# Optimization experiments

Measured on AMD Instinct MI355X. Metric: run time of the kernel, lower is better.

Reference implementation:

```python
import jax, jax.numpy as jnp
import numpy as np

N, E, G, ND, H, C, L = 100000, 640000, 1000, 128, 128, 10, 4
ATOMS_PER_GRAPH = 100  # N = G * ATOMS_PER_GRAPH
NEG_SLOPE = 0.01  # nn.LeakyReLU default


def setup_inputs() -> dict:
    key = jax.random.key(0)
    ks = jax.random.split(key, 16)
    s = 0.05
    return {
        "node_attr": jax.random.normal(ks[0], (N, ND), jnp.float32),
        "edge_index": jax.random.randint(ks[1], (2, E), 0, N, jnp.int64),
        "num_atoms": jnp.full((G,), ATOMS_PER_GRAPH, dtype=jnp.int64),
        "enc_W": jax.random.normal(ks[2], (ND, H), jnp.float32) * s,
        "enc_b": jnp.zeros((H,), jnp.float32),
        "gcn_W": jax.random.normal(ks[3], (L, H, H), jnp.float32) * s,
        "gcn_b": jnp.zeros((L, H), jnp.float32),
        "r_W1": jax.random.normal(ks[4], (H, H), jnp.float32) * s,
        "r_b1": jnp.zeros((H,), jnp.float32),
        "r_W2": jax.random.normal(ks[5], (H, H), jnp.float32) * s,
        "r_b2": jnp.zeros((H,), jnp.float32),
        "s_W1": jax.random.normal(ks[6], (H, H), jnp.float32) * s,
        "s_b1": jnp.zeros((H,), jnp.float32),
        "s_W2": jax.random.normal(ks[7], (H, H), jnp.float32) * s,
        "s_b2": jnp.zeros((H,), jnp.float32),
        "fin_W": jax.random.normal(ks[8], (H, C), jnp.float32) * s,
        "fin_b": jnp.zeros((C,), jnp.float32),
    }


def _leaky(x):
    return jnp.where(x > 0, x, NEG_SLOPE * x)


def reference(node_attr, edge_index, num_atoms, enc_W, enc_b, gcn_W, gcn_b,
              r_W1, r_b1, r_W2, r_b2, s_W1, s_b1, s_W2, s_b2, fin_W, fin_b):
    dst, src = edge_index[0], edge_index[1]
    # degree normalization constant across layers: deg(i) = in-edge count, divide by deg+1
    deg = jax.ops.segment_sum(jnp.ones((E,), node_attr.dtype), dst, num_segments=N)
    inv_deg = 1.0 / (deg + 1.0)  # [N]

    x = node_attr @ enc_W + enc_b  # [N, H]
    for l in range(L):
        h = x @ gcn_W[l] + gcn_b[l]
        agg = jax.ops.segment_sum(h[src], dst, num_segments=N)  # scatter_sum over dst
        x = (h + agg) * inv_deg[:, None]

    # GateMLP: ReLuMLP(x) * SigmoidMLP(x)
    r = _leaky(_leaky(x @ r_W1 + r_b1) @ r_W2 + r_b2)
    g = jax.nn.sigmoid(_leaky(x @ s_W1 + s_b1) @ s_W2 + s_b2)
    x = r * g  # [N, H]

    # graph pooling: scatter_mean over graph ids
    graph_mask = jnp.repeat(jnp.arange(G), num_atoms, total_repeat_length=N)
    gsum = jax.ops.segment_sum(x, graph_mask, num_segments=G)
    cnt = jax.ops.segment_sum(jnp.ones((N,), x.dtype), graph_mask, num_segments=G)
    graph_attr = gsum / jnp.maximum(cnt, 1.0)[:, None]  # [G, H]
    return graph_attr @ fin_W + fin_b  # [G, C]
```

## Files before the change

### kernel.cpp

```cpp
#include <hip/hip_runtime.h>
#include <hip/hip_bf16.h>
#include <cstddef>
#include <cstdint>

#define CAP 32
#define LEAK 0.01f

typedef __attribute__((ext_vector_type(8))) short short8v;
typedef __attribute__((ext_vector_type(4))) float float4v;

__device__ __forceinline__ unsigned short f2bf(float f) {
    uint32_t u = __float_as_uint(f);
    uint32_t r = (u + 0x7FFFu + ((u >> 16) & 1u)) >> 16;
    return (unsigned short)r;
}
__device__ __forceinline__ float bf2f(unsigned short s) {
    return __uint_as_float(((uint32_t)s) << 16);
}
__device__ __forceinline__ short8v frag_from_pairs(uint32_t p0, uint32_t p1,
                                                   uint32_t p2, uint32_t p3) {
    union { uint32_t u[4]; short8v v; } c;
    c.u[0] = p0; c.u[1] = p1; c.u[2] = p2; c.u[3] = p3;
    return c.v;
}

__global__ __launch_bounds__(256) void prep(const int* __restrict__ ei, int E_,
                                            int* __restrict__ cnt,
                                            int* __restrict__ bucket,
                                            const float* __restrict__ node_attr,
                                            unsigned short* __restrict__ bx, int Nn,
                                            const float* __restrict__ enc_W,
                                            const float* __restrict__ gcn_W,
                                            const float* __restrict__ rw1,
                                            const float* __restrict__ rw2,
                                            const float* __restrict__ sw1,
                                            const float* __restrict__ sw2,
                                            const float* __restrict__ enc_b,
                                            const float* __restrict__ gcn_b,
                                            const float* __restrict__ rb1,
                                            const float* __restrict__ sb1,
                                            unsigned short* __restrict__ wpack,
                                            float* __restrict__ fbias,
                                            const int* __restrict__ na,
                                            int* __restrict__ goff, int G_,
                                            int NB_EDGE, int NB_CVT) {
    const int b = blockIdx.x;
    const int tid = threadIdx.x;

    if (b < NB_EDGE) {
        int e = (b * 256 + tid) * 4;
        if (e >= E_) return;
        if (e + 4 <= E_) {
            int4 d4 = *(const int4*)&ei[e];
            int4 s4 = *(const int4*)&ei[(size_t)E_ + e];
            int p0 = atomicAdd(&cnt[d4.x], 1);
            int p1 = atomicAdd(&cnt[d4.y], 1);
            int p2 = atomicAdd(&cnt[d4.z], 1);
            int p3 = atomicAdd(&cnt[d4.w], 1);
            if (p0 < CAP) bucket[(size_t)d4.x * CAP + p0] = s4.x;
            if (p1 < CAP) bucket[(size_t)d4.y * CAP + p1] = s4.y;
            if (p2 < CAP) bucket[(size_t)d4.z * CAP + p2] = s4.z;
            if (p3 < CAP) bucket[(size_t)d4.w * CAP + p3] = s4.w;
        } else {
            for (; e < E_; ++e) {
                int d = ei[e], s = ei[(size_t)E_ + e];
                int p = atomicAdd(&cnt[d], 1);
                if (p < CAP) bucket[(size_t)d * CAP + p] = s;
            }
        }
        return;
    }
    if (b < NB_EDGE + NB_CVT) {
        size_t i8 = ((size_t)(b - NB_EDGE) * 256 + tid) * 8;
        if (i8 < (size_t)Nn * 128) {
            const float* ap = node_attr + i8;
            float4v p = *(const float4v*)ap;
            float4v q = *(const float4v*)(ap + 4);
            short8v v;
            v[0] = (short)f2bf(p[0]); v[1] = (short)f2bf(p[1]);
            v[2] = (short)f2bf(p[2]); v[3] = (short)f2bf(p[3]);
            v[4] = (short)f2bf(q[0]); v[5] = (short)f2bf(q[1]);
            v[6] = (short)f2bf(q[2]); v[7] = (short)f2bf(q[3]);
            *(short8v*)(bx + i8) = v;
        }
        return;
    }
    if (b < NB_EDGE + NB_CVT + 72) {
        int pb = b - (NB_EDGE + NB_CVT);
        int m = pb >> 3;
        if (m == 1) return;
        int idx = (pb & 7) * 256 + tid;
        const float* W;
        switch (m) {
            case 0: W = enc_W; break;
            case 2: case 3: case 4: W = gcn_W + (size_t)(m - 1) * 16384; break;
            case 5: W = rw1; break;
            case 6: W = rw2; break;
            case 7: W = sw1; break;
            default: W = sw2; break;
        }
        int n = idx & 127;
        int fg = (idx >> 7) & 3;
        int kc = idx >> 9;
        short8v v;
#pragma unroll
        for (int j = 0; j < 8; ++j)
            v[j] = (short)f2bf(W[(size_t)(kc * 32 + fg * 8 + j) * 128 + n]);
        *(short8v*)(wpack + (size_t)m * 16384 + (size_t)idx * 8) = v;
        return;
    }
    int fb = b - (NB_EDGE + NB_CVT + 72);
    if (fb < 192) {
        int which = fb / 64;
        int r = (fb % 64) * 2 + (tid >> 7);
        int n = tid & 127;
        const float* A = (which == 0) ? enc_W : gcn_W + (size_t)3 * 16384;
        const float* B = (which == 0) ? gcn_W : ((which == 1) ? rw1 : sw1);
        float acc = 0.f;
#pragma unroll 8
        for (int m2 = 0; m2 < 128; ++m2)
            acc = fmaf(A[(size_t)r * 128 + m2], B[(size_t)m2 * 128 + n], acc);
        int kc = r >> 5, fg2 = (r >> 3) & 3, j = r & 7;
        int sl = (which == 0) ? 1 : ((which == 1) ? 9 : 10);
        wpack[(size_t)sl * 16384 + (size_t)(((kc * 4 + fg2) * 128 + n) * 8 + j)] = f2bf(acc);
    } else if (fb < 195) {
        if (tid < 128) {
            int which = fb - 192;
            const float* B = (which == 0) ? gcn_W : ((which == 1) ? rw1 : sw1);
            const float* ba = (which == 0) ? enc_b : gcn_b + 384;
            const float* bb = (which == 0) ? gcn_b : ((which == 1) ? rb1 : sb1);
            float acc = bb[tid];
            for (int m2 = 0; m2 < 128; ++m2)
                acc = fmaf(ba[m2], B[(size_t)m2 * 128 + tid], acc);
            fbias[which * 128 + tid] = acc;
        }
    } else if (fb == 195) {
        __shared__ int sh[256];
        int base = tid * 4;
        int v0 = (base + 0 < G_) ? na[base + 0] : 0;
        int v1 = (base + 1 < G_) ? na[base + 1] : 0;
        int v2 = (base + 2 < G_) ? na[base + 2] : 0;
        int v3 = (base + 3 < G_) ? na[base + 3] : 0;
        int s = v0 + v1 + v2 + v3;
        sh[tid] = s;
        __syncthreads();
        for (int ofs = 1; ofs < 256; ofs <<= 1) {
            int u = (tid >= ofs) ? sh[tid - ofs] : 0;
            __syncthreads();
            sh[tid] += u;
            __syncthreads();
        }
        int run = sh[tid] - s;
        if (tid == 0) goff[0] = 0;
        run += v0; if (base + 0 < G_) goff[base + 1] = run;
        run += v1; if (base + 1 < G_) goff[base + 2] = run;
        run += v2; if (base + 2 < G_) goff[base + 3] = run;
        run += v3; if (base + 3 < G_) goff[base + 4] = run;
    }
}

__device__ __forceinline__ void load_wf(const unsigned short* __restrict__ Wpack,
                                        int w, int fr, int fg, short8v wf[2][4]) {
    const short8v* Wp = (const short8v*)Wpack;
#pragma unroll
    for (int t = 0; t < 2; ++t)
#pragma unroll
        for (int kc = 0; kc < 4; ++kc)
            wf[t][kc] = Wp[(kc * 4 + fg) * 128 + w * 32 + t * 16 + fr];
}

__device__ __forceinline__ void mfma_tile(const unsigned short* As, int fr, int fg,
                                          const short8v wf[2][4], float4v acc[4][2]) {
#pragma unroll
    for (int m = 0; m < 4; ++m) {
        acc[m][0] = (float4v){0.f, 0.f, 0.f, 0.f};
        acc[m][1] = (float4v){0.f, 0.f, 0.f, 0.f};
    }
#pragma unroll
    for (int kc = 0; kc < 4; ++kc) {
        short8v a[4];
#pragma unroll
        for (int m = 0; m < 4; ++m) {
            int row = m * 16 + fr;
            int cb = (kc * 64 + fg * 16) ^ ((row & 7) << 4);
            a[m] = *(const short8v*)((const char*)As + row * 256 + cb);
        }
#pragma unroll
        for (int m = 0; m < 4; ++m) {
            acc[m][0] = __builtin_amdgcn_mfma_f32_16x16x32_bf16(a[m], wf[0][kc], acc[m][0], 0, 0, 0);
            acc[m][1] = __builtin_amdgcn_mfma_f32_16x16x32_bf16(a[m], wf[1][kc], acc[m][1], 0, 0, 0);
        }
    }
}

__device__ __forceinline__ void acc8(float a[8], uint4 v, float m) {
    a[0] = fmaf(m, bf2f((unsigned short)(v.x & 0xffff)), a[0]);
    a[1] = fmaf(m, bf2f((unsigned short)(v.x >> 16)), a[1]);
    a[2] = fmaf(m, bf2f((unsigned short)(v.y & 0xffff)), a[2]);
    a[3] = fmaf(m, bf2f((unsigned short)(v.y >> 16)), a[3]);
    a[4] = fmaf(m, bf2f((unsigned short)(v.z & 0xffff)), a[4]);
    a[5] = fmaf(m, bf2f((unsigned short)(v.z >> 16)), a[5]);
    a[6] = fmaf(m, bf2f((unsigned short)(v.w & 0xffff)), a[6]);
    a[7] = fmaf(m, bf2f((unsigned short)(v.w >> 16)), a[7]);
}

__device__ __forceinline__ void issue4(const char* __restrict__ xb, int2 prep_,
                                       int gl, int l16, int Nn, int jb, uint4 V[4]) {
    const int sl = gl + (jb >> 1);
    int s0 = __shfl(prep_.x, sl);
    int s1 = __shfl(prep_.y, sl);
    int s2 = __shfl(prep_.x, sl + 1);
    int s3 = __shfl(prep_.y, sl + 1);
    s0 = min(max(s0, 0), Nn - 1);
    s1 = min(max(s1, 0), Nn - 1);
    s2 = min(max(s2, 0), Nn - 1);
    s3 = min(max(s3, 0), Nn - 1);
    V[0] = *(const uint4*)(xb + (size_t)s0 * 256 + l16 * 16);
    V[1] = *(const uint4*)(xb + (size_t)s1 * 256 + l16 * 16);
    V[2] = *(const uint4*)(xb + (size_t)s2 * 256 + l16 * 16);
    V[3] = *(const uint4*)(xb + (size_t)s3 * 256 + l16 * 16);
}

__device__ __forceinline__ void consume4(float a[8], const uint4 V[4], int jb, int d) {
    acc8(a, V[0], (jb + 0 < d) ? 1.f : 0.f);
    acc8(a, V[1], (jb + 1 < d) ? 1.f : 0.f);
    acc8(a, V[2], (jb + 2 < d) ? 1.f : 0.f);
    acc8(a, V[3], (jb + 3 < d) ? 1.f : 0.f);
}

template <bool AGGONLY>
__global__ __launch_bounds__(256, 4) void gcn_fused(const unsigned short* __restrict__ x,
                                                    const int* __restrict__ bucket,
                                                    const int* __restrict__ cnt,
                                                    const unsigned short* __restrict__ Wpack,
                                                    const float* __restrict__ bias,
                                                    unsigned short* __restrict__ xout,
                                                    int Nn) {
    __shared__ unsigned short As[64 * 128];
    const int tid = threadIdx.x;
    const int lane = tid & 63;
    const int w = tid >> 6;
    const int row0 = blockIdx.x * 64;
    const int fr = lane & 15;
    const int fg = lane >> 4;
    const int l16 = lane & 15;
    const int g = lane >> 4;
    const int gl = lane & 48;
    const char* xb = (const char*)x;

    int cfull = 0;
    if (lane < 16) {
        int gn = row0 + w * 16 + lane;
        if (gn >= Nn) gn = Nn - 1;
        cfull = cnt[gn];
    }
    uint4 own[4];
    int2 pre[4];
#pragma unroll
    for (int p = 0; p < 4; ++p) {
        int gn = row0 + w * 16 + p * 4 + g;
        if (gn >= Nn) gn = Nn - 1;
        own[p] = *(const uint4*)(xb + (size_t)gn * 256 + l16 * 16);
        pre[p] = *(const int2*)&bucket[(size_t)gn * CAP + 2 * l16];
    }

#pragma unroll
    for (int p = 0; p < 4; ++p) {
        const int n = p * 4 + g;
        const int r = w * 16 + n;
        const int dfull = __shfl(cfull, n);
        const float id = 1.0f / (float)(dfull + 1);
        const int d = min(dfull, CAP);

        uint4 VA[4], VB[4];
        issue4(xb, pre[p], gl, l16, Nn, 0, VA);

        float a[8];
        {
            uint4 o = own[p];
            a[0] = bf2f((unsigned short)(o.x & 0xffff));
            a[1] = bf2f((unsigned short)(o.x >> 16));
            a[2] = bf2f((unsigned short)(o.y & 0xffff));
            a[3] = bf2f((unsigned short)(o.y >> 16));
            a[4] = bf2f((unsigned short)(o.z & 0xffff));
            a[5] = bf2f((unsigned short)(o.z >> 16));
            a[6] = bf2f((unsigned short)(o.w & 0xffff));
            a[7] = bf2f((unsigned short)(o.w >> 16));
        }

        int j = 0;
        while (true) {
            if (j + 4 < d) issue4(xb, pre[p], gl, l16, Nn, j + 4, VB);
            consume4(a, VA, j, d);
            j += 4;
            if (j >= d) break;
            if (j + 4 < d) issue4(xb, pre[p], gl, l16, Nn, j + 4, VA);
            consume4(a, VB, j, d);
            j += 4;
            if (j >= d) break;
        }

#pragma unroll
        for (int i = 0; i < 8; ++i) a[i] *= id;
        uint4 o;
        o.x = (uint32_t)f2bf(a[0]) | ((uint32_t)f2bf(a[1]) << 16);
        o.y = (uint32_t)f2bf(a[2]) | ((uint32_t)f2bf(a[3]) << 16);
        o.z = (uint32_t)f2bf(a[4]) | ((uint32_t)f2bf(a[5]) << 16);
        o.w = (uint32_t)f2bf(a[6]) | ((uint32_t)f2bf(a[7]) << 16);
        if (AGGONLY) {
            int node = row0 + r;
            if (node < Nn)
                *(uint4*)((char*)xout + (size_t)node * 256 + l16 * 16) = o;
        } else {
            *(uint4*)((char*)As + r * 256 + ((l16 * 16) ^ ((r & 7) << 4))) = o;
        }
    }
    if (AGGONLY) return;

    short8v wf[2][4];
    load_wf(Wpack, w, fr, fg, wf);
    __syncthreads();

    float4v acc[4][2];
    mfma_tile(As, fr, fg, wf, acc);

#pragma unroll
    for (int t = 0; t < 2; ++t) {
        const int col = w * 32 + t * 16 + fr;
        const float bv = bias[col];
#pragma unroll
        for (int m = 0; m < 4; ++m)
#pragma unroll
            for (int q = 0; q < 4; ++q) {
                int row = row0 + m * 16 + fg * 4 + q;
                if (row < Nn) xout[(size_t)row * 128 + col] = f2bf(acc[m][t][q] + bv);
            }
    }
}

__global__ __launch_bounds__(512, 4) void gate_fused(const unsigned short* __restrict__ x,
                                                     const unsigned short* __restrict__ wpack,
                                                     const float* __restrict__ rb1f,
                                                     const float* __restrict__ rb2,
                                                     const float* __restrict__ sb1f,
                                                     const float* __restrict__ sb2,
                                                     unsigned short* __restrict__ out, int M) {
    __shared__ unsigned short Ws[2 * 128 * 128];
    const int tid = threadIdx.x;
    const int lane = tid & 63;
    const int w = tid >> 6;
    const int l16 = lane & 15;
    const int fg = lane >> 4;
    const int row0 = blockIdx.x * 128 + w * 16;

    int xr = row0 + l16;
    if (xr >= M) xr = M - 1;
    short8v xbf[4];
#pragma unroll
    for (int kc = 0; kc < 4; ++kc)
        xbf[kc] = *(const short8v*)(x + (size_t)xr * 128 + kc * 32 + fg * 8);

    const short8v* WL = (const short8v*)Ws;
    uint32_t upR[8][2], upS[8][2];

#define STAGE2(mi0, mi1)                                                      \
    {                                                                         \
        const short8v* s0 = (const short8v*)(wpack + (size_t)(mi0) * 16384);  \
        const short8v* s1 = (const short8v*)(wpack + (size_t)(mi1) * 16384);  \
        short8v* dst = (short8v*)Ws;                                          \
        _Pragma("unroll") for (int i = 0; i < 4; ++i)                         \
            dst[i * 512 + tid] = s0[i * 512 + tid];                          \
        _Pragma("unroll") for (int i = 0; i < 4; ++i)                         \
            dst[2048 + i * 512 + tid] = s1[i * 512 + tid];                    \
    }

#define PASS1(OFS, BIAS, UP)                                                  \
    _Pragma("unroll") for (int nt = 0; nt < 8; ++nt) {                        \
        float4v acc = (float4v){0.f, 0.f, 0.f, 0.f};                          \
        _Pragma("unroll") for (int kc = 0; kc < 4; ++kc)                      \
            acc = __builtin_amdgcn_mfma_f32_16x16x32_bf16(                    \
                WL[(OFS) + (kc * 4 + fg) * 128 + nt * 16 + l16], xbf[kc], acc, 0, 0, 0); \
        _Pragma("unroll") for (int q = 0; q < 4; ++q) {                       \
            float v = acc[q] + (BIAS)[nt * 16 + fg * 4 + q];                  \
            acc[q] = v > 0.f ? v : LEAK * v;                                  \
        }                                                                     \
        UP[nt][0] = (uint32_t)f2bf(acc[0]) | ((uint32_t)f2bf(acc[1]) << 16);  \
        UP[nt][1] = (uint32_t)f2bf(acc[2]) | ((uint32_t)f2bf(acc[3]) << 16);  \
    }

#define MKUF(UP, UF)                                                          \
    _Pragma("unroll") for (int kc = 0; kc < 4; ++kc) {                        \
        uint32_t pr0, pr1, pr2, pr3;                                          \
        {                                                                     \
            int srcl = (((2 * fg + 0) & 3) << 4) + l16;                       \
            uint32_t lo = __shfl((int)UP[2 * kc][0], srcl);                   \
            uint32_t hi = __shfl((int)UP[2 * kc + 1][0], srcl);               \
            pr0 = (fg & 2) ? hi : lo;                                         \
            lo = __shfl((int)UP[2 * kc][1], srcl);                            \
            hi = __shfl((int)UP[2 * kc + 1][1], srcl);                        \
            pr1 = (fg & 2) ? hi : lo;                                         \
        }                                                                     \
        {                                                                     \
            int srcl = (((2 * fg + 1) & 3) << 4) + l16;                       \
            uint32_t lo = __shfl((int)UP[2 * kc][0], srcl);                   \
            uint32_t hi = __shfl((int)UP[2 * kc + 1][0], srcl);               \
            pr2 = (fg & 2) ? hi : lo;                                         \
            lo = __shfl((int)UP[2 * kc][1], srcl);                            \
            hi = __shfl((int)UP[2 * kc + 1][1], srcl);                        \
            pr3 = (fg & 2) ? hi : lo;                                         \
        }                                                                     \
        UF[kc] = frag_from_pairs(pr0, pr1, pr2, pr3);                         \
    }

    STAGE2(9, 10);
    __syncthreads();
    PASS1(0, rb1f, upR);
    PASS1(2048, sb1f, upS);
    __syncthreads();

    STAGE2(6, 8);
    __syncthreads();

    short8v uf[4];
    MKUF(upR, uf);
    float4v rf[8];
#pragma unroll
    for (int t2 = 0; t2 < 8; ++t2) {
        float4v acc = (float4v){0.f, 0.f, 0.f, 0.f};
#pragma unroll
        for (int kc = 0; kc < 4; ++kc)
            acc = __builtin_amdgcn_mfma_f32_16x16x32_bf16(
                uf[kc], WL[(kc * 4 + fg) * 128 + t2 * 16 + l16], acc, 0, 0, 0);
        const float bv = rb2[t2 * 16 + l16];
#pragma unroll
        for (int q = 0; q < 4; ++q) {
            float v = acc[q] + bv;
            rf[t2][q] = v > 0.f ? v : LEAK * v;
        }
    }

    MKUF(upS, uf);
#pragma unroll
    for (int t2 = 0; t2 < 8; ++t2) {
        float4v acc = (float4v){0.f, 0.f, 0.f, 0.f};
#pragma unroll
        for (int kc = 0; kc < 4; ++kc)
            acc = __builtin_amdgcn_mfma_f32_16x16x32_bf16(
                uf[kc], WL[2048 + (kc * 4 + fg) * 128 + t2 * 16 + l16], acc, 0, 0, 0);
        const float bv = sb2[t2 * 16 + l16];
#pragma unroll
        for (int q = 0; q < 4; ++q) {
            int row = row0 + fg * 4 + q;
            if (row < M) {
                float gg = 1.f / (1.f + __expf(-(acc[q] + bv)));
                out[(size_t)row * 128 + t2 * 16 + l16] = f2bf(gg * rf[t2][q]);
            }
        }
    }
#undef STAGE2
#undef PASS1
#undef MKUF
}

__global__ void pool(const unsigned short* __restrict__ x, const int* __restrict__ goff,
                     float* __restrict__ gattr, int G_) {
    int g = blockIdx.x * 2 + (threadIdx.x >> 7);
    if (g >= G_) return;
    int d = threadIdx.x & 127;
    int a0 = goff[g], a1 = goff[g + 1];
    float s0 = 0.f, s1 = 0.f, s2 = 0.f, s3 = 0.f;
    int a = a0;
    for (; a + 4 <= a1; a += 4) {
        s0 += bf2f(__builtin_nontemporal_load(&x[(size_t)(a + 0) * 128 + d]));
        s1 += bf2f(__builtin_nontemporal_load(&x[(size_t)(a + 1) * 128 + d]));
        s2 += bf2f(__builtin_nontemporal_load(&x[(size_t)(a + 2) * 128 + d]));
        s3 += bf2f(__builtin_nontemporal_load(&x[(size_t)(a + 3) * 128 + d]));
    }
    for (; a < a1; ++a) s0 += bf2f(__builtin_nontemporal_load(&x[(size_t)a * 128 + d]));
    float s = (s0 + s1) + (s2 + s3);
    float c = (float)max(a1 - a0, 1);
    gattr[(size_t)g * 128 + d] = s / c;
}

__global__ void final_gemm(const float* __restrict__ gattr, const float* __restrict__ fW,
                           const float* __restrict__ fb, float* __restrict__ out,
                           int G_, int C_) {
    int i = blockIdx.x * 256 + threadIdx.x;
    if (i >= G_ * C_) return;
    int g = i / C_, c = i % C_;
    const float* row = gattr + (size_t)g * 128;
    float s = fb[c];
    for (int k = 0; k < 128; ++k) s = fmaf(row[k], fW[k * C_ + c], s);
    out[i] = s;
}

extern "C" void kernel_launch(void* const* d_in, const int* in_sizes, int n_in,
                              void* d_out, int out_size, void* d_ws, size_t ws_size,
                              hipStream_t stream) {
    const float* node_attr = (const float*)d_in[0];
    const int* edge_index  = (const int*)d_in[1];
    const int* num_atoms   = (const int*)d_in[2];
    const float* enc_W = (const float*)d_in[3];
    const float* enc_b = (const float*)d_in[4];
    const float* gcn_W = (const float*)d_in[5];
    const float* gcn_b = (const float*)d_in[6];
    const float* r_W1 = (const float*)d_in[7];
    const float* r_b1 = (const float*)d_in[8];
    const float* r_W2 = (const float*)d_in[9];
    const float* r_b2 = (const float*)d_in[10];
    const float* s_W1 = (const float*)d_in[11];
    const float* s_b1 = (const float*)d_in[12];
    const float* s_W2 = (const float*)d_in[13];
    const float* s_b2 = (const float*)d_in[14];
    const float* fin_W = (const float*)d_in[15];
    const float* fin_b = (const float*)d_in[16];
    float* out = (float*)d_out;

    const int N_ = in_sizes[0] / 128;
    const int E_ = in_sizes[1] / 2;
    const int G_ = in_sizes[2];
    const int C_ = in_sizes[16];

    size_t off = 0;
    auto alloc = [&](size_t bytes) -> void* {
        void* p = (char*)d_ws + off;
        off += (bytes + 255) & ~(size_t)255;
        return p;
    };
    unsigned short* bx = (unsigned short*)alloc((size_t)N_ * 128 * 2);
    unsigned short* bh = (unsigned short*)alloc((size_t)N_ * 128 * 2);
    int* bucket = (int*)alloc((size_t)N_ * CAP * 4);
    int* cnt    = (int*)alloc((size_t)N_ * 4);
    unsigned short* wpack = (unsigned short*)alloc((size_t)11 * 16384 * 2);
    float* fbias = (float*)alloc((size_t)3 * 128 * 4);
    int* goff   = (int*)alloc((size_t)(G_ + 1) * 4);
    float* gattr = (float*)alloc((size_t)G_ * 128 * 4);
    (void)ws_size; (void)n_in; (void)out_size;

    const int gemm_grid = (N_ + 63) / 64;
    const int NB_EDGE = (E_ / 4 + 255) / 256;
    const int NB_CVT = (N_ * 16 + 255) / 256;
    const int NB_PREP = NB_EDGE + NB_CVT + 72 + 196;

    hipMemsetAsync(cnt, 0, (size_t)N_ * 4, stream);
    prep<<<NB_PREP, 256, 0, stream>>>(edge_index, E_, cnt, bucket,
                                      node_attr, bx, N_,
                                      enc_W, gcn_W, r_W1, r_W2, s_W1, s_W2,
                                      enc_b, gcn_b, r_b1, s_b1,
                                      wpack, fbias, num_atoms, goff, G_,
                                      NB_EDGE, NB_CVT);

    gcn_fused<false><<<gemm_grid, 256, 0, stream>>>(bx, bucket, cnt,
                                                    wpack + (size_t)1 * 16384, fbias, bh, N_);
    gcn_fused<false><<<gemm_grid, 256, 0, stream>>>(bh, bucket, cnt,
                                                    wpack + (size_t)2 * 16384, gcn_b + 128, bx, N_);
    gcn_fused<false><<<gemm_grid, 256, 0, stream>>>(bx, bucket, cnt,
                                                    wpack + (size_t)3 * 16384, gcn_b + 256, bh, N_);
    gcn_fused<true><<<gemm_grid, 256, 0, stream>>>(bh, bucket, cnt,
                                                   nullptr, nullptr, bx, N_);

    gate_fused<<<(N_ + 127) / 128, 512, 0, stream>>>(bx, wpack, fbias + 128, r_b2,
                                                     fbias + 256, s_b2, bh, N_);

    pool<<<(G_ + 1) / 2, 256, 0, stream>>>(bh, goff, gattr, G_);
    final_gemm<<<(G_ * C_ + 255) / 256, 256, 0, stream>>>(gattr, fin_W, fin_b, out, G_, C_);
}
```

Before: 267.6 us.

## Fold all GCN layer weights into gate first-layer weights, aggregate-only passes

Since aggregation and degree scaling are linear and commute with the right-multiplication by weights, the change composes enc_W and all four gcn_W into the gate MLP first-layer weights (plus the bias chain) inside a single prep block using MFMA. The per-layer GEMMs are dropped from the four propagation kernels, which now only aggregate the raw bf16 inputs. This removes four N×128×128 GEMMs, at the cost of a serial single-block weight-folding chain inside prep and extra bf16 rounding in the folded weights. Bias handling needs care: the bias propagates through the aggregation with degree-dependent scaling, which the constant-bias fold may not capture exactly.

```diff
diff --git a/kernel.cpp b/kernel.cpp
--- a/kernel.cpp
+++ b/kernel.cpp
@@ -17,11 +17,55 @@
 __device__ __forceinline__ float bf2f(unsigned short s) {
     return __uint_as_float(((uint32_t)s) << 16);
 }
-__device__ __forceinline__ short8v frag_from_pairs(uint32_t p0, uint32_t p1,
-                                                   uint32_t p2, uint32_t p3) {
-    union { uint32_t u[4]; short8v v; } c;
-    c.u[0] = p0; c.u[1] = p1; c.u[2] = p2; c.u[3] = p3;
-    return c.v;
+
+__device__ __forceinline__ void load_wf(const unsigned short* __restrict__ Wpack,
+                                        int w, int fr, int fg, short8v wf[2][4]) {
+    const short8v* Wp = (const short8v*)Wpack;
+#pragma unroll
+    for (int t = 0; t < 2; ++t)
+#pragma unroll
+        for (int kc = 0; kc < 4; ++kc)
+            wf[t][kc] = Wp[(kc * 4 + fg) * 128 + w * 32 + t * 16 + fr];
+}
+
+__device__ __forceinline__ void load_wf_f32(const float* __restrict__ W,
+                                            int w, int fr, int fg, short8v wf[2][4]) {
+#pragma unroll
+    for (int t = 0; t < 2; ++t) {
+        const int n = w * 32 + t * 16 + fr;
+#pragma unroll
+        for (int kc = 0; kc < 4; ++kc) {
+            short8v v;
+#pragma unroll
+            for (int j = 0; j < 8; ++j)
+                v[j] = (short)f2bf(W[(size_t)(kc * 32 + fg * 8 + j) * 128 + n]);
+            wf[t][kc] = v;
+        }
+    }
+}
+
+__device__ __forceinline__ void mfma_tile(const unsigned short* As, int fr, int fg,
+                                          const short8v wf[2][4], float4v acc[4][2]) {
+#pragma unroll
+    for (int m = 0; m < 4; ++m) {
+        acc[m][0] = (float4v){0.f, 0.f, 0.f, 0.f};
+        acc[m][1] = (float4v){0.f, 0.f, 0.f, 0.f};
+    }
+#pragma unroll
+    for (int kc = 0; kc < 4; ++kc) {
+        short8v a[4];
+#pragma unroll
+        for (int m = 0; m < 4; ++m) {
+            int row = m * 16 + fr;
+            int cb = (kc * 64 + fg * 16) ^ ((row & 7) << 4);
+            a[m] = *(const short8v*)((const char*)As + row * 256 + cb);
+        }
+#pragma unroll
+        for (int m = 0; m < 4; ++m) {
+            acc[m][0] = __builtin_amdgcn_mfma_f32_16x16x32_bf16(a[m], wf[0][kc], acc[m][0], 0, 0, 0);
+            acc[m][1] = __builtin_amdgcn_mfma_f32_16x16x32_bf16(a[m], wf[1][kc], acc[m][1], 0, 0, 0);
+        }
+    }
 }
 
 __global__ __launch_bounds__(256) void prep(const int* __restrict__ ei, int E_,
@@ -40,6 +84,7 @@
                                             const float* __restrict__ rb1,
                                             const float* __restrict__ sb1,
                                             unsigned short* __restrict__ wpack,
+                                            unsigned short* __restrict__ foldbuf,
                                             float* __restrict__ fbias,
                                             const int* __restrict__ na,
                                             int* __restrict__ goff, int G_,
@@ -88,17 +133,9 @@
     if (b < NB_EDGE + NB_CVT + 72) {
         int pb = b - (NB_EDGE + NB_CVT);
         int m = pb >> 3;
-        if (m == 1) return;
+        if (m != 6 && m != 8) return;
         int idx = (pb & 7) * 256 + tid;
-        const float* W;
-        switch (m) {
-            case 0: W = enc_W; break;
-            case 2: case 3: case 4: W = gcn_W + (size_t)(m - 1) * 16384; break;
-            case 5: W = rw1; break;
-            case 6: W = rw2; break;
-            case 7: W = sw1; break;
-            default: W = sw2; break;
-        }
+        const float* W = (m == 6) ? rw2 : sw2;
         int n = idx & 127;
         int fg = (idx >> 7) & 3;
         int kc = idx >> 9;
@@ -110,31 +147,100 @@
         return;
     }
     int fb = b - (NB_EDGE + NB_CVT + 72);
-    if (fb < 192) {
-        int which = fb / 64;
-        int r = (fb % 64) * 2 + (tid >> 7);
-        int n = tid & 127;
-        const float* A = (which == 0) ? enc_W : gcn_W + (size_t)3 * 16384;
-        const float* B = (which == 0) ? gcn_W : ((which == 1) ? rw1 : sw1);
-        float acc = 0.f;
-#pragma unroll 8
-        for (int m2 = 0; m2 < 128; ++m2)
-            acc = fmaf(A[(size_t)r * 128 + m2], B[(size_t)m2 * 128 + n], acc);
-        int kc = r >> 5, fg2 = (r >> 3) & 3, j = r & 7;
-        int sl = (which == 0) ? 1 : ((which == 1) ? 9 : 10);
-        wpack[(size_t)sl * 16384 + (size_t)(((kc * 4 + fg2) * 128 + n) * 8 + j)] = f2bf(acc);
-    } else if (fb < 195) {
+    if (fb == 0) {
+        __shared__ unsigned short As[64 * 128];
+        __shared__ float betaL[128];
+
+        if (tid < 128) betaL[tid] = enc_b[tid];
+        __syncthreads();
+        for (int l = 0; l < 4; ++l) {
+            const float* Wl = gcn_W + (size_t)l * 16384;
+            float acc = 0.f;
+            if (tid < 128) {
+                acc = gcn_b[l * 128 + tid];
+                for (int k = 0; k < 128; ++k)
+                    acc = fmaf(betaL[k], Wl[(size_t)k * 128 + tid], acc);
+            }
+            __syncthreads();
+            if (tid < 128) betaL[tid] = acc;
+            __syncthreads();
+        }
         if (tid < 128) {
-            int which = fb - 192;
-            const float* B = (which == 0) ? gcn_W : ((which == 1) ? rw1 : sw1);
-            const float* ba = (which == 0) ? enc_b : gcn_b + 384;
-            const float* bb = (which == 0) ? gcn_b : ((which == 1) ? rb1 : sb1);
-            float acc = bb[tid];
-            for (int m2 = 0; m2 < 128; ++m2)
-                acc = fmaf(ba[m2], B[(size_t)m2 * 128 + tid], acc);
-            fbias[which * 128 + tid] = acc;
-        }
-    } else if (fb == 195) {
+            float a1 = rb1[tid], a2 = sb1[tid];
+            for (int k = 0; k < 128; ++k) {
+                float bk = betaL[k];
+                a1 = fmaf(bk, rw1[(size_t)k * 128 + tid], a1);
+                a2 = fmaf(bk, sw1[(size_t)k * 128 + tid], a2);
+            }
+            fbias[128 + tid] = a1;
+            fbias[256 + tid] = a2;
+        }
+        __syncthreads();
+
+        const int lane = tid & 63;
+        const int w = tid >> 6;
+        const int fr = lane & 15;
+        const int fg = lane >> 4;
+        unsigned short* f0 = foldbuf;
+        unsigned short* f1 = foldbuf + 32768;
+        const float* Ls[5] = {gcn_W + (size_t)3 * 16384, gcn_W + (size_t)2 * 16384,
+                              gcn_W + (size_t)1 * 16384, gcn_W, enc_W};
+
+        for (int p = 0; p < 5; ++p) {
+            const unsigned short* inb = (p == 0) ? nullptr : (((p - 1) & 1) == 0 ? f0 : f1);
+            unsigned short* outb = (p == 4) ? (wpack + (size_t)9 * 16384)
+                                            : ((p & 1) == 0 ? f0 : f1);
+            const float* Lp = Ls[p];
+#pragma unroll 1
+            for (int rt = 0; rt < 2; ++rt) {
+                {
+                    const int r = tid >> 2;
+                    const int cg = tid & 3;
+                    const float* Ap = Lp + (size_t)(rt * 64 + r) * 128 + cg * 32;
+                    char* lbase = (char*)As + r * 256;
+#pragma unroll
+                    for (int i = 0; i < 4; ++i) {
+                        float4v pv = *(const float4v*)(Ap + i * 8);
+                        float4v qv = *(const float4v*)(Ap + i * 8 + 4);
+                        short8v v;
+                        v[0] = (short)f2bf(pv[0]); v[1] = (short)f2bf(pv[1]);
+                        v[2] = (short)f2bf(pv[2]); v[3] = (short)f2bf(pv[3]);
+                        v[4] = (short)f2bf(qv[0]); v[5] = (short)f2bf(qv[1]);
+                        v[6] = (short)f2bf(qv[2]); v[7] = (short)f2bf(qv[3]);
+                        int cb = (cg * 64 + i * 16) ^ ((r & 7) << 4);
+                        *(short8v*)(lbase + cb) = v;
+                    }
+                }
+                __syncthreads();
+
+#pragma unroll 1
+                for (int panel = 0; panel < 2; ++panel) {
+                    short8v wf[2][4];
+                    if (p == 0) load_wf_f32(panel ? sw1 : rw1, w, fr, fg, wf);
+                    else        load_wf(inb + panel * 16384, w, fr, fg, wf);
+                    float4v acc[4][2];
+                    mfma_tile(As, fr, fg, wf, acc);
+                    unsigned short* dstp = outb + panel * 16384;
+#pragma unroll
+                    for (int t = 0; t < 2; ++t)
+#pragma unroll
+                        for (int m = 0; m < 4; ++m)
+#pragma unroll
+                            for (int q = 0; q < 4; ++q) {
+                                int r = rt * 64 + m * 16 + fg * 4 + q;
+                                int c = w * 32 + t * 16 + fr;
+                                dstp[(size_t)((((r >> 5) * 4 + ((r >> 3) & 3)) * 128 + c) * 8)
+                                     + (r & 7)] = f2bf(acc[m][t][q]);
+                            }
+                }
+                __syncthreads();
+            }
+            __threadfence();
+            __syncthreads();
+        }
+        return;
+    }
+    if (fb == 1) {
         __shared__ int sh[256];
         int base = tid * 4;
         int v0 = (base + 0 < G_) ? na[base + 0] : 0;
@@ -156,40 +262,6 @@
         run += v1; if (base + 1 < G_) goff[base + 2] = run;
         run += v2; if (base + 2 < G_) goff[base + 3] = run;
         run += v3; if (base + 3 < G_) goff[base + 4] = run;
-    }
-}
-
-__device__ __forceinline__ void load_wf(const unsigned short* __restrict__ Wpack,
-                                        int w, int fr, int fg, short8v wf[2][4]) {
-    const short8v* Wp = (const short8v*)Wpack;
-#pragma unroll
-    for (int t = 0; t < 2; ++t)
-#pragma unroll
-        for (int kc = 0; kc < 4; ++kc)
-            wf[t][kc] = Wp[(kc * 4 + fg) * 128 + w * 32 + t * 16 + fr];
-}
-
-__device__ __forceinline__ void mfma_tile(const unsigned short* As, int fr, int fg,
-                                          const short8v wf[2][4], float4v acc[4][2]) {
-#pragma unroll
-    for (int m = 0; m < 4; ++m) {
-        acc[m][0] = (float4v){0.f, 0.f, 0.f, 0.f};
-        acc[m][1] = (float4v){0.f, 0.f, 0.f, 0.f};
-    }
-#pragma unroll
-    for (int kc = 0; kc < 4; ++kc) {
-        short8v a[4];
-#pragma unroll
-        for (int m = 0; m < 4; ++m) {
-            int row = m * 16 + fr;
-            int cb = (kc * 64 + fg * 16) ^ ((row & 7) << 4);
-            a[m] = *(const short8v*)((const char*)As + row * 256 + cb);
-        }
-#pragma unroll
-        for (int m = 0; m < 4; ++m) {
-            acc[m][0] = __builtin_amdgcn_mfma_f32_16x16x32_bf16(a[m], wf[0][kc], acc[m][0], 0, 0, 0);
-            acc[m][1] = __builtin_amdgcn_mfma_f32_16x16x32_bf16(a[m], wf[1][kc], acc[m][1], 0, 0, 0);
-        }
     }
 }
 
@@ -228,21 +300,15 @@
     acc8(a, V[3], (jb + 3 < d) ? 1.f : 0.f);
 }
 
-template <bool AGGONLY>
-__global__ __launch_bounds__(256, 4) void gcn_fused(const unsigned short* __restrict__ x,
-                                                    const int* __restrict__ bucket,
-                                                    const int* __restrict__ cnt,
-                                                    const unsigned short* __restrict__ Wpack,
-                                                    const float* __restrict__ bias,
-                                                    unsigned short* __restrict__ xout,
-                                                    int Nn) {
-    __shared__ unsigned short As[64 * 128];
+__global__ __launch_bounds__(256, 4) void agg_pass(const unsigned short* __restrict__ x,
+                                                   const int* __restrict__ bucket,
+                                                   const int* __restrict__ cnt,
+                                                   unsigned short* __restrict__ xout,
+                                                   int Nn) {
     const int tid = threadIdx.x;
     const int lane = tid & 63;
     const int w = tid >> 6;
     const int row0 = blockIdx.x * 64;
-    const int fr = lane & 15;
-    const int fg = lane >> 4;
     const int l16 = lane & 15;
     const int g = lane >> 4;
     const int gl = lane & 48;
@@ -307,34 +373,9 @@
         o.y = (uint32_t)f2bf(a[2]) | ((uint32_t)f2bf(a[3]) << 16);
         o.z = (uint32_t)f2bf(a[4]) | ((uint32_t)f2bf(a[5]) << 16);
         o.w = (uint32_t)f2bf(a[6]) | ((uint32_t)f2bf(a[7]) << 16);
-        if (AGGONLY) {
-            int node = row0 + r;
-            if (node < Nn)
-                *(uint4*)((char*)xout + (size_t)node * 256 + l16 * 16) = o;
-        } else {
-            *(uint4*)((char*)As + r * 256 + ((l16 * 16) ^ ((r & 7) << 4))) = o;
-        }
-    }
-    if (AGGONLY) return;
-
-    short8v wf[2][4];
-    load_wf(Wpack, w, fr, fg, wf);
-    __syncthreads();
-
-    float4v acc[4][2];
-    mfma_tile(As, fr, fg, wf, acc);
-
-#pragma unroll
-    for (int t = 0; t < 2; ++t) {
-        const int col = w * 32 + t * 16 + fr;
-        const float bv = bias[col];
-#pragma unroll
-        for (int m = 0; m < 4; ++m)
-#pragma unroll
-            for (int q = 0; q < 4; ++q) {
-                int row = row0 + m * 16 + fg * 4 + q;
-                if (row < Nn) xout[(size_t)row * 128 + col] = f2bf(acc[m][t][q] + bv);
-            }
+        int node = row0 + r;
+        if (node < Nn)
+            *(uint4*)((char*)xout + (size_t)node * 256 + l16 * 16) = o;
     }
 }
 
@@ -362,6 +403,8 @@
 
     const short8v* WL = (const short8v*)Ws;
     uint32_t upR[8][2], upS[8][2];
+
+    union { uint32_t u[4]; short8v v; } cvt;
 
 #define STAGE2(mi0, mi1)                                                      \
     {                                                                         \
@@ -409,7 +452,8 @@
             hi = __shfl((int)UP[2 * kc + 1][1], srcl);                        \
             pr3 = (fg & 2) ? hi : lo;                                         \
         }                                                                     \
-        UF[kc] = frag_from_pairs(pr0, pr1, pr2, pr3);                         \
+        cvt.u[0] = pr0; cvt.u[1] = pr1; cvt.u[2] = pr2; cvt.u[3] = pr3;       \
+        UF[kc] = cvt.v;                                                       \
     }
 
     STAGE2(9, 10);
@@ -532,32 +576,29 @@
     int* bucket = (int*)alloc((size_t)N_ * CAP * 4);
     int* cnt    = (int*)alloc((size_t)N_ * 4);
     unsigned short* wpack = (unsigned short*)alloc((size_t)11 * 16384 * 2);
+    unsigned short* foldbuf = (unsigned short*)alloc((size_t)2 * 32768 * 2);
     float* fbias = (float*)alloc((size_t)3 * 128 * 4);
     int* goff   = (int*)alloc((size_t)(G_ + 1) * 4);
     float* gattr = (float*)alloc((size_t)G_ * 128 * 4);
     (void)ws_size; (void)n_in; (void)out_size;
 
-    const int gemm_grid = (N_ + 63) / 64;
+    const int agg_grid = (N_ + 63) / 64;
     const int NB_EDGE = (E_ / 4 + 255) / 256;
     const int NB_CVT = (N_ * 16 + 255) / 256;
-    const int NB_PREP = NB_EDGE + NB_CVT + 72 + 196;
+    const int NB_PREP = NB_EDGE + NB_CVT + 72 + 2;
 
     hipMemsetAsync(cnt, 0, (size_t)N_ * 4, stream);
     prep<<<NB_PREP, 256, 0, stream>>>(edge_index, E_, cnt, bucket,
                                       node_attr, bx, N_,
                                       enc_W, gcn_W, r_W1, r_W2, s_W1, s_W2,
                                       enc_b, gcn_b, r_b1, s_b1,
-                                      wpack, fbias, num_atoms, goff, G_,
+                                      wpack, foldbuf, fbias, num_atoms, goff, G_,
                                       NB_EDGE, NB_CVT);
 
-    gcn_fused<false><<<gemm_grid, 256, 0, stream>>>(bx, bucket, cnt,
-                                                    wpack + (size_t)1 * 16384, fbias, bh, N_);
-    gcn_fused<false><<<gemm_grid, 256, 0, stream>>>(bh, bucket, cnt,
-                                                    wpack + (size_t)2 * 16384, gcn_b + 128, bx, N_);
-    gcn_fused<false><<<gemm_grid, 256, 0, stream>>>(bx, bucket, cnt,
-                                                    wpack + (size_t)3 * 16384, gcn_b + 256, bh, N_);
-    gcn_fused<true><<<gemm_grid, 256, 0, stream>>>(bh, bucket, cnt,
-                                                   nullptr, nullptr, bx, N_);
+    agg_pass<<<agg_grid, 256, 0, stream>>>(bx, bucket, cnt, bh, N_);
+    agg_pass<<<agg_grid, 256, 0, stream>>>(bh, bucket, cnt, bx, N_);
+    agg_pass<<<agg_grid, 256, 0, stream>>>(bx, bucket, cnt, bh, N_);
+    agg_pass<<<agg_grid, 256, 0, stream>>>(bh, bucket, cnt, bx, N_);
 
     gate_fused<<<(N_ + 127) / 128, 512, 0, stream>>>(bx, wpack, fbias + 128, r_b2,
                                                      fbias + 256, s_b2, bh, N_);
```

After: 293.7 us. +9.8%, slower.
